# Optimization experiments

Hardware: AMD Instinct MI355X
Metric: run time of the kernel (lower is better)

## Reference

```python
import jax, jax.numpy as jnp
import numpy as np
from jax import lax

B, CIN, H, W = 64, 3, 64, 64
HID = 128          # hidden_dim == embedding_dim
K = 1024           # num_embeddings
BETA = 0.25        # commitment cost


def _conv(x, w, b, stride):
    # torch Conv2d, padding=0, NCHW / OIHW weights
    y = lax.conv_general_dilated(x, w, (stride, stride), 'VALID',
                                 dimension_numbers=('NCHW', 'OIHW', 'NCHW'))
    return y + b[None, :, None, None]


def _conv_transpose(x, w, b, stride):
    # torch ConvTranspose2d, padding=0; w is [Cin, Cout, kh, kw] (torch layout)
    kh, kw = w.shape[2], w.shape[3]
    w2 = jnp.flip(w, (2, 3)).transpose(1, 0, 2, 3)  # -> OIHW, spatially flipped
    y = lax.conv_general_dilated(x, w2, (1, 1),
                                 [(kh - 1, kh - 1), (kw - 1, kw - 1)],
                                 lhs_dilation=(stride, stride),
                                 dimension_numbers=('NCHW', 'OIHW', 'NCHW'))
    return y + b[None, :, None, None]


def setup_inputs() -> dict:
    key = jax.random.key(0)
    ks = jax.random.split(key, 10)
    s = 0.05
    return {
        'x':      jax.random.normal(ks[0], (B, CIN, H, W), jnp.float32),
        'enc_w1': jax.random.normal(ks[1], (HID, CIN, 4, 4), jnp.float32) * s,
        'enc_b1': jnp.zeros((HID,), jnp.float32),
        'enc_w2': jax.random.normal(ks[2], (HID, HID, 2, 2), jnp.float32) * s,
        'enc_b2': jnp.zeros((HID,), jnp.float32),
        'codebook': jax.random.uniform(ks[3], (K, HID), jnp.float32,
                                       minval=-1.0 / K, maxval=1.0 / K),
        'dec_w1': jax.random.normal(ks[4], (HID, HID, 2, 2), jnp.float32) * s,
        'dec_b1': jnp.zeros((HID,), jnp.float32),
        'dec_w2': jax.random.normal(ks[5], (HID, CIN, 4, 4), jnp.float32) * s,
        'dec_b2': jnp.zeros((CIN,), jnp.float32),
    }


def reference(x, enc_w1, enc_b1, enc_w2, enc_b2, codebook,
              dec_w1, dec_b1, dec_w2, dec_b2):
    # ---- encoder ----
    z = jax.nn.relu(_conv(x, enc_w1, enc_b1, 2))
    z = jax.nn.relu(_conv(z, enc_w2, enc_b2, 1))   # [B, HID, 30, 30]

    # ---- vector quantizer (faithful to torch reshape semantics) ----
    D = HID
    flat = z.reshape(-1, D)                        # [N, D], C-order rows
    # squared euclidean distances (argmin identical to torch.cdist argmin)
    d2 = (jnp.sum(flat * flat, axis=1, keepdims=True)
          - 2.0 * flat @ codebook.T
          + jnp.sum(codebook * codebook, axis=1)[None, :])  # [N, K]
    idx = jnp.argmin(d2, axis=1)                   # [N]
    quantized = codebook[idx].reshape(z.shape)

    e_latent = jnp.mean((lax.stop_gradient(quantized) - z) ** 2)
    q_latent = jnp.mean((quantized - lax.stop_gradient(z)) ** 2)
    loss = q_latent + BETA * e_latent

    q_st = z + lax.stop_gradient(quantized - z)    # straight-through

    n = flat.shape[0]
    avg_probs = jnp.zeros((K,), z.dtype).at[idx].add(1.0) / n
    perplexity = jnp.exp(-jnp.sum(avg_probs * jnp.log(avg_probs + 1e-10)))

    # ---- decoder ----
    y = jax.nn.relu(_conv_transpose(q_st, dec_w1, dec_b1, 1))
    x_recon = _conv_transpose(y, dec_w2, dec_b2, 2)  # [B, 3, 64, 64]
    return x_recon, loss, perplexity
```

## Files before the change

### kernel.cpp

```cpp
#include <hip/hip_runtime.h>

#define B_    64
#define CIN_  3
#define HW_   64
#define HID_  128
#define K_    1024
#define H1_   31
#define H2_   30
#define NROWS_ 57600
#define NELEM_ 7372800

typedef __bf16 bf16_t;
typedef __attribute__((ext_vector_type(8))) __bf16 bf16x8;
typedef __attribute__((ext_vector_type(4))) float f32x4;
typedef __attribute__((ext_vector_type(16))) float f32x16;

__global__ __launch_bounds__(256) void wprep_k(const float* __restrict__ ew1,
    const float* __restrict__ ew2, const float* __restrict__ dw1,
    const float* __restrict__ dw2, const float* __restrict__ cb,
    bf16_t* __restrict__ wc1, bf16_t* __restrict__ wc2,
    bf16_t* __restrict__ wd1, bf16_t* __restrict__ wt2,
    bf16_t* __restrict__ cbb, float* __restrict__ cnorm,
    unsigned* __restrict__ hist, float* __restrict__ sse) {
  int id = blockIdx.x * 256 + threadIdx.x;
  int t = id >> 14, co = (id >> 7) & 127, ci = id & 127;
  wc2[id] = (bf16_t)ew2[(co * 128 + ci) * 4 + t];
  wd1[id] = (bf16_t)dw1[(ci * 128 + co) * 4 + (3 - t)];
  if (id < 8192) {
    int n = id >> 9, k = id & 511;
    int tap = k >> 7, c = k & 127;
    if (n < 12) {
      int nco = n >> 2, ph = (n >> 1) & 1, pw = n & 1;
      int off = (tap >> 1) * 8 + (tap & 1) * 2;
      wt2[id] = (bf16_t)dw2[c * 48 + nco * 16 + ph * 4 + pw + off];
    } else {
      wt2[id] = (bf16_t)0.f;
    }
    int c1 = id >> 6, k1 = id & 63;
    wc1[id] = (bf16_t)(k1 < 48 ? ew1[c1 * 48 + k1] : 0.f);
  }
  if (id < K_) {
    float s0 = 0.f;
    for (int d = 0; d < HID_; d += 4) {
      float4 v = *(const float4*)&cb[id * HID_ + d];
      bf16_t tt[4] = {(bf16_t)v.x, (bf16_t)v.y, (bf16_t)v.z, (bf16_t)v.w};
      *(ushort4*)&((ushort*)cbb)[id * HID_ + d] = *(ushort4*)tt;
      float f0 = (float)tt[0], f1 = (float)tt[1];
      float f2 = (float)tt[2], f3 = (float)tt[3];
      s0 += f0 * f0 + f1 * f1 + f2 * f2 + f3 * f3;
    }
    cnorm[id] = s0;
    hist[id] = 0u;
  }
  if (id == 0) *sse = 0.f;
}

__global__ __launch_bounds__(256, 2) void conv1m_k(const float* __restrict__ x,
    const bf16_t* __restrict__ wc1, const float* __restrict__ bias,
    ushort* __restrict__ z1t) {
  __shared__ __align__(16) bf16_t as_[64 * 72];
  __shared__ __align__(16) bf16_t bs_[128 * 72];
  int b = blockIdx.x >> 4, rt = blockIdx.x & 15;
  int tid = threadIdx.x, wv = tid >> 6, ln = tid & 63;
  const float* xb = x + (size_t)b * 12288;
  #pragma unroll
  for (int it = 0; it < 16; ++it) {
    int e = it * 256 + tid;
    int p = e >> 6, k = e & 63;
    float v = 0.f;
    if (k < 48) {
      int ci = k >> 4, kh = (k >> 2) & 3, kw = k & 3;
      int row = 2 * rt + (p >> 5); if (row > 30) row = 30;
      int col = p & 31;            if (col > 30) col = 30;
      v = xb[ci * 4096 + (2 * row + kh) * 64 + 2 * col + kw];
    }
    as_[p * 72 + k] = (bf16_t)v;
  }
  {
    const float4* wg = (const float4*)wc1;
    #pragma unroll
    for (int it = 0; it < 4; ++it) {
      int fi = it * 256 + tid;
      int co = fi >> 3, k8 = fi & 7;
      *(float4*)&bs_[co * 72 + k8 * 8] = wg[fi];
    }
  }
  __syncthreads();
  int q = ln >> 4, l = ln & 15;
  f32x4 acc8[8];
  #pragma unroll
  for (int c = 0; c < 8; ++c) acc8[c] = (f32x4){0.f, 0.f, 0.f, 0.f};
  bf16x8 af[2];
  #pragma unroll
  for (int kk = 0; kk < 2; ++kk)
    af[kk] = *(const bf16x8*)&as_[(wv * 16 + l) * 72 + kk * 32 + q * 8];
  #pragma unroll
  for (int cot = 0; cot < 8; ++cot) {
    #pragma unroll
    for (int kk = 0; kk < 2; ++kk) {
      bf16x8 bf = *(const bf16x8*)&bs_[(cot * 16 + l) * 72 + kk * 32 + q * 8];
      acc8[cot] = __builtin_amdgcn_mfma_f32_16x16x32_bf16(af[kk], bf,
                                                          acc8[cot], 0, 0, 0);
    }
  }
  #pragma unroll
  for (int cot = 0; cot < 8; ++cot) {
    int co = cot * 16 + l;
    float bv = bias[co];
    #pragma unroll
    for (int r = 0; r < 4; ++r) {
      int pos = wv * 16 + q * 4 + r;
      int prow = 2 * rt + (pos >> 5), pcol = pos & 31;
      if (prow < 31 && pcol < 31) {
        float v = fmaxf(acc8[cot][r] + bv, 0.f);
        bf16_t h = (bf16_t)v;
        z1t[((size_t)(b * 1024 + prow * 32 + pcol)) * 128 + co] = *(ushort*)&h;
      }
    }
  }
}

__global__ __launch_bounds__(256, 2) void conv2m_k(const bf16_t* __restrict__ z1t,
    const bf16_t* __restrict__ wc2, const float* __restrict__ bias,
    ushort* __restrict__ zbuf) {
  __shared__ __align__(16) bf16_t as_[98 * 136];
  __shared__ __align__(16) bf16_t bs_[128 * 136];
  int blk = blockIdx.x;
  int b = blk / 15, rt = blk % 15;
  int tid = threadIdx.x, wv = tid >> 6, ln = tid & 63;
  const float4* src = (const float4*)(z1t + ((size_t)b * 1024 + rt * 64) * 128);
  #pragma unroll
  for (int s = 0; s < 7; ++s) {
    int f = s * 256 + tid;
    if (f < 1568) {
      int lp = f >> 4, c16 = f & 15;
      *(float4*)&as_[lp * 136 + c16 * 8] = src[f];
    }
  }
  int m = wv * 16 + (ln & 15), q = ln >> 4;
  f32x4 acc8[8];
  #pragma unroll
  for (int c = 0; c < 8; ++c) acc8[c] = (f32x4){0.f, 0.f, 0.f, 0.f};
  const float4* w4 = (const float4*)wc2;
  #pragma unroll
  for (int t = 0; t < 4; ++t) {
    __syncthreads();
    #pragma unroll
    for (int s = 0; s < 8; ++s) {
      int f = s * 256 + tid;
      int co = f >> 4, c16 = f & 15;
      *(float4*)&bs_[co * 136 + c16 * 8] = w4[t * 2048 + f];
    }
    __syncthreads();
    int off = (t >> 1) * 32 + (t & 1);
    bf16x8 af[4];
    #pragma unroll
    for (int kk = 0; kk < 4; ++kk)
      af[kk] = *(const bf16x8*)&as_[(m + off) * 136 + kk * 32 + q * 8];
    #pragma unroll
    for (int cot = 0; cot < 8; ++cot) {
      #pragma unroll
      for (int kk = 0; kk < 4; ++kk) {
        bf16x8 bf = *(const bf16x8*)&bs_[(cot * 16 + (ln & 15)) * 136 +
                                         kk * 32 + q * 8];
        acc8[cot] = __builtin_amdgcn_mfma_f32_16x16x32_bf16(af[kk], bf,
                                                            acc8[cot], 0, 0, 0);
      }
    }
  }
  #pragma unroll
  for (int cot = 0; cot < 8; ++cot) {
    int co = cot * 16 + (ln & 15);
    float bv = bias[co];
    #pragma unroll
    for (int r = 0; r < 4; ++r) {
      int mo = wv * 16 + q * 4 + r;
      int ocol = mo & 31;
      if (ocol < 30) {
        int orow = rt * 2 + (mo >> 5);
        float v = fmaxf(acc8[cot][r] + bv, 0.f);
        bf16_t h = (bf16_t)v;
        zbuf[(size_t)(b * HID_ + co) * 900 + orow * 30 + ocol] = *(ushort*)&h;
      }
    }
  }
}

__global__ __launch_bounds__(256, 2) void vq1_k(const bf16_t* __restrict__ zb,
    const bf16_t* __restrict__ cbb, const float* __restrict__ cnorm,
    int* __restrict__ idxArr, unsigned* __restrict__ hist,
    float* __restrict__ sse) {
  __shared__ __align__(16) bf16_t zs[64 * 136];
  __shared__ __align__(16) bf16_t cbs[128 * 136];
  __shared__ float cns[K_];
  __shared__ unsigned long long red2[128];
  int n0 = blockIdx.x * 64;
  int tid = threadIdx.x;
  int wv = tid >> 6, ln = tid & 63;
  {
    const float4* zg4 = (const float4*)(zb + (size_t)n0 * HID_);
    #pragma unroll
    for (int s = 0; s < 4; ++s) {
      int f = s * 256 + tid;
      int row = f >> 4, seg = f & 15;
      *(float4*)&zs[row * 136 + seg * 8] = zg4[f];
    }
    ((float4*)cns)[tid] = ((const float4*)cnorm)[tid];
  }
  __syncthreads();
  int mt = wv & 1, npair = wv >> 1;
  int lr = ln & 31, lh = ln >> 5;
  bf16x8 afr[8];
  #pragma unroll
  for (int ks = 0; ks < 8; ++ks)
    afr[ks] = *(const bf16x8*)&zs[(mt * 32 + lr) * 136 + ks * 16 + lh * 8];
  unsigned long long best[16];
  #pragma unroll
  for (int r = 0; r < 16; ++r) best[r] = ~0ull;
  const float4* cg4 = (const float4*)cbb;
  for (int c0 = 0; c0 < K_; c0 += 128) {
    __syncthreads();
    #pragma unroll
    for (int s = 0; s < 8; ++s) {
      int f = s * 256 + tid;
      int code = f >> 4, seg = f & 15;
      *(float4*)&cbs[code * 136 + seg * 8] = cg4[(c0 + code) * 16 + seg];
    }
    __syncthreads();
    #pragma unroll
    for (int nt2 = 0; nt2 < 2; ++nt2) {
      int nt = npair * 2 + nt2;
      f32x16 acc = {0.f, 0.f, 0.f, 0.f, 0.f, 0.f, 0.f, 0.f,
                    0.f, 0.f, 0.f, 0.f, 0.f, 0.f, 0.f, 0.f};
      #pragma unroll
      for (int ks = 0; ks < 8; ++ks) {
        bf16x8 bfr = *(const bf16x8*)&cbs[(nt * 32 + lr) * 136 +
                                          ks * 16 + lh * 8];
        acc = __builtin_amdgcn_mfma_f32_32x32x16_bf16(afr[ks], bfr, acc,
                                                      0, 0, 0);
      }
      int code = c0 + nt * 32 + lr;
      float cn = cns[code];
      unsigned long long lc = (unsigned)code;
      #pragma unroll
      for (int r = 0; r < 16; ++r) {
        float dist = cn - 2.f * acc[r];
        unsigned u = __float_as_uint(dist);
        u = (u & 0x80000000u) ? ~u : (u | 0x80000000u);
        unsigned long long p = ((unsigned long long)u << 32) | lc;
        if (p < best[r]) best[r] = p;
      }
    }
  }
  #pragma unroll
  for (int r = 0; r < 16; ++r) {
    unsigned long long b = best[r];
    #pragma unroll
    for (int o = 16; o > 0; o >>= 1) {
      unsigned long long ob = __shfl_xor(b, o, 64);
      if (ob < b) b = ob;
    }
    best[r] = b;
  }
  if (lr == 0) {
    #pragma unroll
    for (int r = 0; r < 16; ++r)
      red2[((mt * 2 + npair) * 2 + lh) * 16 + r] = best[r];
  }
  __syncthreads();
  if (tid < 64) {
    int fmt = tid >> 5, r32 = tid & 31;
    int half = (r32 >> 2) & 1;
    int reg = (r32 & 3) | (((r32 >> 3) & 3) << 2);
    unsigned long long b0 = red2[((fmt * 2 + 0) * 2 + half) * 16 + reg];
    unsigned long long b1 = red2[((fmt * 2 + 1) * 2 + half) * 16 + reg];
    unsigned long long b = (b1 < b0) ? b1 : b0;
    int bi = (int)(b & 0xffffffffu);
    idxArr[n0 + tid] = bi;
    atomicAdd(&hist[bi], 1u);
    unsigned hi = (unsigned)(b >> 32);
    unsigned orig = (hi & 0x80000000u) ? (hi & 0x7fffffffu) : ~hi;
    float dmin = __uint_as_float(orig);
    float zn = 0.f;
    #pragma unroll
    for (int s = 0; s < 16; ++s) {
      bf16x8 v = *(const bf16x8*)&zs[tid * 136 + s * 8];
      #pragma unroll
      for (int e = 0; e < 8; ++e) {
        float fv = (float)v[e];
        zn = fmaf(fv, fv, zn);
      }
    }
    float se = zn + dmin;
    #pragma unroll
    for (int o = 32; o > 0; o >>= 1) se += __shfl_down(se, o, 64);
    if (tid == 0) atomicAdd(sse, se);
  }
}

__global__ __launch_bounds__(256) void tqz_k(const bf16_t* __restrict__ cbb,
    const int* __restrict__ idxArr, ushort* __restrict__ qt) {
  __shared__ ushort t[60 * 128];
  int bid = blockIdx.x, tid = threadIdx.x;
  if (bid < 960) {
    int b = bid / 15, st = bid % 15;
    int s0 = st * 60;
    #pragma unroll
    for (int it = 0; it < 8; ++it) {
      int task = it * 256 + tid;
      if (task < 1920) {
        int sc = task >> 7, c = task & 127;
        int f = b * 115200 + c * 900 + s0 + sc * 4;
        int n = f >> 7, d = f & 127;
        int k = idxArr[n];
        ushort4 v = *(const ushort4*)((const ushort*)cbb + k * 128 + d);
        t[(sc * 4 + 0) * 128 + c] = v.x;
        t[(sc * 4 + 1) * 128 + c] = v.y;
        t[(sc * 4 + 2) * 128 + c] = v.z;
        t[(sc * 4 + 3) * 128 + c] = v.w;
      }
    }
    __syncthreads();
    #pragma unroll
    for (int it = 0; it < 4; ++it) {
      int task = it * 256 + tid;
      if (task < 960) {
        int sl = task >> 4, c16 = task & 15;
        int s = s0 + sl;
        int h = s / 30, w = s - h * 30;
        int p = (h + 1) * 32 + (w + 1);
        *(uint4*)&qt[((size_t)(b * 1024 + p)) * 128 + c16 * 8] =
            *(uint4*)&t[sl * 128 + c16 * 8];
      }
    }
  } else {
    int zb_ = (bid - 960) * 4;
    uint4 zz = {0u, 0u, 0u, 0u};
    for (int e = tid; e < 4 * 124 * 16; e += 256) {
      int bb = zb_ + e / (124 * 16);
      int rem = e % (124 * 16);
      int pe = rem >> 4, s16 = rem & 15;
      int p;
      if (pe < 32) p = pe;
      else if (pe < 64) p = 31 * 32 + (pe - 32);
      else {
        int idx = pe - 64;
        p = (1 + (idx >> 1)) * 32 + ((idx & 1) ? 31 : 0);
      }
      *(uint4*)&qt[((size_t)(bb * 1024 + p)) * 128 + s16 * 8] = zz;
    }
  }
}

__global__ __launch_bounds__(256, 2) void convt1m_k(const bf16_t* __restrict__ qt,
    const bf16_t* __restrict__ wd1, const float* __restrict__ bias,
    ushort* __restrict__ yt) {
  __shared__ __align__(16) bf16_t as_[98 * 136];
  __shared__ __align__(16) bf16_t bs_[128 * 136];
  int blk = blockIdx.x;
  int b = blk >> 4, rt = blk & 15;
  int tid = threadIdx.x, wv = tid >> 6, ln = tid & 63;
  {
    uint4 zz = {0u, 0u, 0u, 0u};
    ushort* ytb = yt + (size_t)b * 1156 * 128;
    int nrows = (rt < 15) ? 2 : 1;
    int r0 = 2 * rt + 1;
    for (int e = tid; e < nrows * 48; e += 256) {
      int rr = e / 48, rem = e % 48, cc = rem / 16, s16 = rem % 16;
      int col = (cc == 0) ? 0 : (cc == 1 ? 32 : 33);
      *(uint4*)&ytb[((size_t)((r0 + rr) * 34 + col)) * 128 + s16 * 8] = zz;
    }
    if (rt == 0)
      for (int e = tid; e < 34 * 16; e += 256)
        *(uint4*)&ytb[((size_t)(e >> 4)) * 128 + (e & 15) * 8] = zz;
    if (rt == 15)
      for (int e = tid; e < 2 * 34 * 16; e += 256) {
        int rr = 32 + e / 544, rem = e % 544;
        *(uint4*)&ytb[((size_t)(rr * 34 + (rem >> 4))) * 128 + (rem & 15) * 8]
            = zz;
      }
  }
  const float4* src = (const float4*)(qt + (size_t)b * 1024 * 128);
  #pragma unroll
  for (int s = 0; s < 7; ++s) {
    int f = s * 256 + tid;
    if (f < 1568) {
      int lp = f >> 4, c16 = f & 15;
      int gr = rt * 64 + lp;
      if (gr > 1023) gr = 1023;
      *(float4*)&as_[lp * 136 + c16 * 8] = src[gr * 16 + c16];
    }
  }
  int m = wv * 16 + (ln & 15), q = ln >> 4;
  f32x4 acc8[8];
  #pragma unroll
  for (int c = 0; c < 8; ++c) acc8[c] = (f32x4){0.f, 0.f, 0.f, 0.f};
  const float4* w4 = (const float4*)wd1;
  #pragma unroll
  for (int t = 0; t < 4; ++t) {
    __syncthreads();
    #pragma unroll
    for (int s = 0; s < 8; ++s) {
      int f = s * 256 + tid;
      int co = f >> 4, c16 = f & 15;
      *(float4*)&bs_[co * 136 + c16 * 8] = w4[t * 2048 + f];
    }
    __syncthreads();
    int off = (t >> 1) * 32 + (t & 1);
    bf16x8 af[4];
    #pragma unroll
    for (int kk = 0; kk < 4; ++kk)
      af[kk] = *(const bf16x8*)&as_[(m + off) * 136 + kk * 32 + q * 8];
    #pragma unroll
    for (int cot = 0; cot < 8; ++cot) {
      #pragma unroll
      for (int kk = 0; kk < 4; ++kk) {
        bf16x8 bf = *(const bf16x8*)&bs_[(cot * 16 + (ln & 15)) * 136 +
                                         kk * 32 + q * 8];
        acc8[cot] = __builtin_amdgcn_mfma_f32_16x16x32_bf16(af[kk], bf,
                                                            acc8[cot], 0, 0, 0);
      }
    }
  }
  #pragma unroll
  for (int cot = 0; cot < 8; ++cot) {
    int co = cot * 16 + (ln & 15);
    float bv = bias[co];
    #pragma unroll
    for (int r = 0; r < 4; ++r) {
      int mo = wv * 16 + q * 4 + r;
      int orow = rt * 2 + (mo >> 5), ocol = mo & 31;
      if (orow < 31 && ocol < 31) {
        float v = fmaxf(acc8[cot][r] + bv, 0.f);
        bf16_t h = (bf16_t)v;
        yt[((size_t)b * 1156 + (orow + 1) * 34 + (ocol + 1)) * 128 + co] =
            *(ushort*)&h;
      }
    }
  }
}

__global__ __launch_bounds__(256, 2) void convt2m_k(const bf16_t* __restrict__ yt,
    const bf16_t* __restrict__ wt2, const float* __restrict__ bias,
    const unsigned* __restrict__ hist, const float* __restrict__ sse,
    float* __restrict__ out) {
  __shared__ __align__(16) bf16_t as_[128 * 136];
  __shared__ float redf[256];
  int b = blockIdx.x >> 4, rt = blockIdx.x & 15;
  int tid = threadIdx.x, wv = tid >> 6, ln = tid & 63;
  const float4* src = (const float4*)(yt + ((size_t)b * 1156 + rt * 68) * 128);
  #pragma unroll
  for (int s = 0; s < 8; ++s) {
    int f = s * 256 + tid;
    int lp = f >> 4, c16 = f & 15;
    *(float4*)&as_[lp * 136 + c16 * 8] = src[f];
  }
  __syncthreads();
  int mloc = wv * 16 + (ln & 15), q = ln >> 4;
  int qh = mloc >> 5, qw = mloc & 31;
  int base = (qh + 1) * 34 + qw + 1;
  f32x4 acc = {0.f, 0.f, 0.f, 0.f};
  #pragma unroll
  for (int kc = 0; kc < 16; ++kc) {
    int tap = kc >> 2;
    int toff = (tap & 1) + (tap >> 1) * 34;
    bf16x8 af = *(const bf16x8*)&as_[(base - toff) * 136 +
                                     (kc & 3) * 32 + q * 8];
    bf16x8 bf = *(const bf16x8*)&wt2[(size_t)(ln & 15) * 512 + kc * 32 + q * 8];
    acc = __builtin_amdgcn_mfma_f32_16x16x32_bf16(af, bf, acc, 0, 0, 0);
  }
  __syncthreads();
  float* bb = (float*)as_;
  #pragma unroll
  for (int r = 0; r < 4; ++r)
    bb[(wv * 16 + q * 4 + r) * 16 + (ln & 15)] = acc[r];
  __syncthreads();
  if (tid < 192) {
    int row_id = tid >> 4;
    int co = row_id >> 2, ohoff = row_id & 3;
    int qhl = ohoff >> 1, ph = ohoff & 1;
    float bv = bias[co];
    int ow0 = (tid & 15) * 4;
    float tmp[4];
    #pragma unroll
    for (int e = 0; e < 4; ++e) {
      int ow = ow0 + e;
      tmp[e] = bb[(qhl * 32 + (ow >> 1)) * 16 + co * 4 + ph * 2 + (ow & 1)]
               + bv;
    }
    *(float4*)&out[((size_t)(b * 3 + co)) * 4096 + (rt * 4 + ohoff) * 64 + ow0]
        = *(float4*)tmp;
  }
  if (blockIdx.x == 0) {
    float e = 0.f;
    for (int k = tid; k < K_; k += 256) {
      float p = (float)hist[k] * (1.0f / (float)NROWS_);
      e += p * logf(p + 1e-10f);
    }
    redf[tid] = e;
    __syncthreads();
    #pragma unroll
    for (int t = 128; t > 0; t >>= 1) {
      if (tid < t) redf[tid] += redf[tid + t];
      __syncthreads();
    }
    if (tid == 0) {
      out[786432] = 1.25f * (*sse) * (1.0f / (float)NELEM_);
      out[786433] = expf(-redf[0]);
    }
  }
}

extern "C" void kernel_launch(void* const* d_in, const int* in_sizes, int n_in,
                              void* d_out, int out_size, void* d_ws,
                              size_t ws_size, hipStream_t stream) {
  (void)in_sizes; (void)n_in; (void)out_size; (void)ws_size;
  const float* x   = (const float*)d_in[0];
  const float* ew1 = (const float*)d_in[1];
  const float* eb1 = (const float*)d_in[2];
  const float* ew2 = (const float*)d_in[3];
  const float* eb2 = (const float*)d_in[4];
  const float* cb  = (const float*)d_in[5];
  const float* dw1 = (const float*)d_in[6];
  const float* db1 = (const float*)d_in[7];
  const float* dw2 = (const float*)d_in[8];
  const float* db2 = (const float*)d_in[9];
  float* out = (float*)d_out;
  char* ws = (char*)d_ws;

  ushort*   yt    = (ushort*)(ws);
  bf16_t*   z1t   = (bf16_t*)(ws + 65175552);
  bf16_t*   qt    = (bf16_t*)(ws + 65175552);
  ushort*   zbuf  = (ushort*)(ws + 81985536);
  bf16_t*   cbb   = (bf16_t*)(ws + 96731136);
  bf16_t*   wc2   = (bf16_t*)(ws + 96993280);
  bf16_t*   wd1   = (bf16_t*)(ws + 97124352);
  int*      idxArr= (int*)(ws + 97255424);
  unsigned* hist  = (unsigned*)(ws + 97485824);
  float*    cnorm = (float*)(ws + 97489920);
  float*    sse   = (float*)(ws + 97494016);
  bf16_t*   wt2   = (bf16_t*)(ws + 97497088);
  bf16_t*   wc1   = (bf16_t*)(ws + 97513472);

  wprep_k<<<dim3(256), dim3(256), 0, stream>>>(ew1, ew2, dw1, dw2, cb,
                                               wc1, wc2, wd1, wt2,
                                               cbb, cnorm, hist, sse);
  conv1m_k<<<dim3(1024), dim3(256), 0, stream>>>(x, wc1, eb1, (ushort*)z1t);
  conv2m_k<<<dim3(960), dim3(256), 0, stream>>>(z1t, wc2, eb2, zbuf);
  vq1_k<<<dim3(900), dim3(256), 0, stream>>>((const bf16_t*)zbuf, cbb, cnorm,
                                             idxArr, hist, sse);
  tqz_k<<<dim3(976), dim3(256), 0, stream>>>(cbb, idxArr, (ushort*)qt);
  convt1m_k<<<dim3(1024), dim3(256), 0, stream>>>(qt, wd1, db1, yt);
  convt2m_k<<<dim3(1024), dim3(256), 0, stream>>>((const bf16_t*)yt, wt2, db2,
                                                  hist, sse, out);
}
```

Baseline: 230.4 us.

## Enlarge VQ tile to 128 rows, prefetch codebook into registers, simplify argmin

The VQ distance kernel now handles 128 rows per block instead of 64, so each codebook tile loaded into shared memory is reused across twice as many rows, and the grid halves to 450 blocks. The next codebook chunk is prefetched into registers while the current one is computed. The 64-bit packed argmin is replaced by a float max of dot minus half the code norm, with explicit index tie-breaking. The cost is more registers per thread and more shared memory, and the fewer, larger blocks may leave some compute units idle.

```diff
diff --git a/kernel.cpp b/kernel.cpp
--- a/kernel.cpp
+++ b/kernel.cpp
@@ -190,111 +190,133 @@
     const bf16_t* __restrict__ cbb, const float* __restrict__ cnorm,
     int* __restrict__ idxArr, unsigned* __restrict__ hist,
     float* __restrict__ sse) {
-  __shared__ __align__(16) bf16_t zs[64 * 136];
+  __shared__ __align__(16) bf16_t zs[128 * 136];
   __shared__ __align__(16) bf16_t cbs[128 * 136];
   __shared__ float cns[K_];
-  __shared__ unsigned long long red2[128];
-  int n0 = blockIdx.x * 64;
+  __shared__ float redS[256];
+  __shared__ int   redI[256];
+  int n0 = blockIdx.x * 128;
   int tid = threadIdx.x;
   int wv = tid >> 6, ln = tid & 63;
+  int lr = ln & 31, lh = ln >> 5;
+  int mtp = wv >> 1, ntp = wv & 1;
   {
     const float4* zg4 = (const float4*)(zb + (size_t)n0 * HID_);
     #pragma unroll
-    for (int s = 0; s < 4; ++s) {
-      int f = s * 256 + tid;
-      int row = f >> 4, seg = f & 15;
-      *(float4*)&zs[row * 136 + seg * 8] = zg4[f];
-    }
-    ((float4*)cns)[tid] = ((const float4*)cnorm)[tid];
-  }
-  __syncthreads();
-  int mt = wv & 1, npair = wv >> 1;
-  int lr = ln & 31, lh = ln >> 5;
-  bf16x8 afr[8];
-  #pragma unroll
-  for (int ks = 0; ks < 8; ++ks)
-    afr[ks] = *(const bf16x8*)&zs[(mt * 32 + lr) * 136 + ks * 16 + lh * 8];
-  unsigned long long best[16];
-  #pragma unroll
-  for (int r = 0; r < 16; ++r) best[r] = ~0ull;
-  const float4* cg4 = (const float4*)cbb;
-  for (int c0 = 0; c0 < K_; c0 += 128) {
-    __syncthreads();
-    #pragma unroll
     for (int s = 0; s < 8; ++s) {
       int f = s * 256 + tid;
-      int code = f >> 4, seg = f & 15;
-      *(float4*)&cbs[code * 136 + seg * 8] = cg4[(c0 + code) * 16 + seg];
-    }
-    __syncthreads();
+      *(float4*)&zs[(f >> 4) * 136 + (f & 15) * 8] = zg4[f];
+    }
+    float4 cv = ((const float4*)cnorm)[tid];
+    cv.x *= 0.5f; cv.y *= 0.5f; cv.z *= 0.5f; cv.w *= 0.5f;
+    ((float4*)cns)[tid] = cv;
+  }
+  const float4* cg4 = (const float4*)cbb;
+  float4 pf[8];
+  #pragma unroll
+  for (int s = 0; s < 8; ++s) pf[s] = cg4[s * 256 + tid];
+  __syncthreads();
+  bf16x8 af0[8], af1[8];
+  #pragma unroll
+  for (int ks = 0; ks < 8; ++ks) {
+    af0[ks] = *(const bf16x8*)&zs[(mtp * 64 + lr) * 136 + ks * 16 + lh * 8];
+    af1[ks] = *(const bf16x8*)&zs[(mtp * 64 + 32 + lr) * 136 +
+                                  ks * 16 + lh * 8];
+  }
+  float bS0[16], bS1[16];
+  int   bI0[16], bI1[16];
+  #pragma unroll
+  for (int r = 0; r < 16; ++r) {
+    bS0[r] = -3.4e38f; bS1[r] = -3.4e38f; bI0[r] = 0; bI1[r] = 0;
+  }
+  for (int c0 = 0; c0 < K_; c0 += 128) {
+    __syncthreads();
+    #pragma unroll
+    for (int s = 0; s < 8; ++s) {
+      int f = s * 256 + tid;
+      *(float4*)&cbs[(f >> 4) * 136 + (f & 15) * 8] = pf[s];
+    }
+    __syncthreads();
+    if (c0 + 128 < K_) {
+      #pragma unroll
+      for (int s = 0; s < 8; ++s)
+        pf[s] = cg4[(c0 + 128) * 16 + s * 256 + tid];
+    }
     #pragma unroll
     for (int nt2 = 0; nt2 < 2; ++nt2) {
-      int nt = npair * 2 + nt2;
-      f32x16 acc = {0.f, 0.f, 0.f, 0.f, 0.f, 0.f, 0.f, 0.f,
-                    0.f, 0.f, 0.f, 0.f, 0.f, 0.f, 0.f, 0.f};
+      int nt = ntp * 2 + nt2;
+      int code = c0 + nt * 32 + lr;
+      float hcn = cns[code];
+      f32x16 a0 = {0.f, 0.f, 0.f, 0.f, 0.f, 0.f, 0.f, 0.f,
+                   0.f, 0.f, 0.f, 0.f, 0.f, 0.f, 0.f, 0.f};
+      f32x16 a1 = {0.f, 0.f, 0.f, 0.f, 0.f, 0.f, 0.f, 0.f,
+                   0.f, 0.f, 0.f, 0.f, 0.f, 0.f, 0.f, 0.f};
       #pragma unroll
       for (int ks = 0; ks < 8; ++ks) {
         bf16x8 bfr = *(const bf16x8*)&cbs[(nt * 32 + lr) * 136 +
                                           ks * 16 + lh * 8];
-        acc = __builtin_amdgcn_mfma_f32_32x32x16_bf16(afr[ks], bfr, acc,
-                                                      0, 0, 0);
-      }
-      int code = c0 + nt * 32 + lr;
-      float cn = cns[code];
-      unsigned long long lc = (unsigned)code;
+        a0 = __builtin_amdgcn_mfma_f32_32x32x16_bf16(af0[ks], bfr, a0, 0, 0, 0);
+        a1 = __builtin_amdgcn_mfma_f32_32x32x16_bf16(af1[ks], bfr, a1, 0, 0, 0);
+      }
       #pragma unroll
       for (int r = 0; r < 16; ++r) {
-        float dist = cn - 2.f * acc[r];
-        unsigned u = __float_as_uint(dist);
-        u = (u & 0x80000000u) ? ~u : (u | 0x80000000u);
-        unsigned long long p = ((unsigned long long)u << 32) | lc;
-        if (p < best[r]) best[r] = p;
+        float s0 = a0[r] - hcn;
+        if (s0 > bS0[r]) { bS0[r] = s0; bI0[r] = code; }
+        float s1 = a1[r] - hcn;
+        if (s1 > bS1[r]) { bS1[r] = s1; bI1[r] = code; }
       }
     }
   }
   #pragma unroll
   for (int r = 0; r < 16; ++r) {
-    unsigned long long b = best[r];
+    float s0 = bS0[r]; int i0 = bI0[r];
+    float s1 = bS1[r]; int i1 = bI1[r];
     #pragma unroll
     for (int o = 16; o > 0; o >>= 1) {
-      unsigned long long ob = __shfl_xor(b, o, 64);
-      if (ob < b) b = ob;
-    }
-    best[r] = b;
+      float os = __shfl_xor(s0, o, 64); int oi = __shfl_xor(i0, o, 64);
+      if (os > s0 || (os == s0 && oi < i0)) { s0 = os; i0 = oi; }
+      os = __shfl_xor(s1, o, 64); oi = __shfl_xor(i1, o, 64);
+      if (os > s1 || (os == s1 && oi < i1)) { s1 = os; i1 = oi; }
+    }
+    bS0[r] = s0; bI0[r] = i0; bS1[r] = s1; bI1[r] = i1;
   }
   if (lr == 0) {
-    #pragma unroll
-    for (int r = 0; r < 16; ++r)
-      red2[((mt * 2 + npair) * 2 + lh) * 16 + r] = best[r];
+    int base0 = ((mtp * 2 + 0) * 4 + ntp * 2 + lh) * 16;
+    int base1 = ((mtp * 2 + 1) * 4 + ntp * 2 + lh) * 16;
+    #pragma unroll
+    for (int r = 0; r < 16; ++r) {
+      redS[base0 + r] = bS0[r]; redI[base0 + r] = bI0[r];
+      redS[base1 + r] = bS1[r]; redI[base1 + r] = bI1[r];
+    }
   }
   __syncthreads();
-  if (tid < 64) {
-    int fmt = tid >> 5, r32 = tid & 31;
+  if (tid < 128) {
+    int mtg = tid >> 5, r32 = tid & 31;
     int half = (r32 >> 2) & 1;
     int reg = (r32 & 3) | (((r32 >> 3) & 3) << 2);
-    unsigned long long b0 = red2[((fmt * 2 + 0) * 2 + half) * 16 + reg];
-    unsigned long long b1 = red2[((fmt * 2 + 1) * 2 + half) * 16 + reg];
-    unsigned long long b = (b1 < b0) ? b1 : b0;
-    int bi = (int)(b & 0xffffffffu);
+    int e0 = (mtg * 4 + half) * 16 + reg;
+    int e1 = (mtg * 4 + 2 + half) * 16 + reg;
+    float s0 = redS[e0], s1 = redS[e1];
+    int b0 = redI[e0], b1 = redI[e1];
+    bool t = (s1 > s0) || (s1 == s0 && b1 < b0);
+    float sbest = t ? s1 : s0;
+    int bi = t ? b1 : b0;
     idxArr[n0 + tid] = bi;
     atomicAdd(&hist[bi], 1u);
-    unsigned hi = (unsigned)(b >> 32);
-    unsigned orig = (hi & 0x80000000u) ? (hi & 0x7fffffffu) : ~hi;
-    float dmin = __uint_as_float(orig);
     float zn = 0.f;
     #pragma unroll
-    for (int s = 0; s < 16; ++s) {
-      bf16x8 v = *(const bf16x8*)&zs[tid * 136 + s * 8];
+    for (int sg = 0; sg < 16; ++sg) {
+      bf16x8 v = *(const bf16x8*)&zs[tid * 136 + sg * 8];
       #pragma unroll
       for (int e = 0; e < 8; ++e) {
         float fv = (float)v[e];
         zn = fmaf(fv, fv, zn);
       }
     }
-    float se = zn + dmin;
+    float se = zn - 2.f * sbest;
     #pragma unroll
     for (int o = 32; o > 0; o >>= 1) se += __shfl_down(se, o, 64);
-    if (tid == 0) atomicAdd(sse, se);
+    if (ln == 0) atomicAdd(sse, se);
   }
 }
 
@@ -547,7 +569,7 @@
                                                cbb, cnorm, hist, sse);
   conv1m_k<<<dim3(1024), dim3(256), 0, stream>>>(x, wc1, eb1, (ushort*)z1t);
   conv2m_k<<<dim3(960), dim3(256), 0, stream>>>(z1t, wc2, eb2, zbuf);
-  vq1_k<<<dim3(900), dim3(256), 0, stream>>>((const bf16_t*)zbuf, cbb, cnorm,
+  vq1_k<<<dim3(450), dim3(256), 0, stream>>>((const bf16_t*)zbuf, cbb, cnorm,
                                              idxArr, hist, sse);
   tqz_k<<<dim3(976), dim3(256), 0, stream>>>(cbb, idxArr, (ushort*)qt);
   convt1m_k<<<dim3(1024), dim3(256), 0, stream>>>(qt, wd1, db1, yt);
```

Result: slower. 248.0 us (+7.6%).

## Restructure VQ argmin to stream codebook from global into registers, drop LDS tiles

Applied to the files above, without the earlier changes.

The VQ kernel now gives each wave 32 full rows against all 1024 codes. Codebook fragments are loaded straight from global (L2-resident) into registers with double buffering, replacing the LDS staging and its block barriers. The accumulator is seeded with -0.5*||c||^2 so argmin becomes an argmax on float score plus index, dropping the 64-bit packed compare. Blocks handle 128 rows, so half as many blocks each do more work, which could reduce occupancy or parallelism and puts more load on the cache through repeated codebook reads.

```diff
diff --git a/kernel.cpp b/kernel.cpp
--- a/kernel.cpp
+++ b/kernel.cpp
@@ -190,111 +190,113 @@
     const bf16_t* __restrict__ cbb, const float* __restrict__ cnorm,
     int* __restrict__ idxArr, unsigned* __restrict__ hist,
     float* __restrict__ sse) {
-  __shared__ __align__(16) bf16_t zs[64 * 136];
-  __shared__ __align__(16) bf16_t cbs[128 * 136];
   __shared__ float cns[K_];
-  __shared__ unsigned long long red2[128];
-  int n0 = blockIdx.x * 64;
+  __shared__ float redS[128];
+  __shared__ int   redI[128];
+  int n0 = blockIdx.x * 128;
   int tid = threadIdx.x;
   int wv = tid >> 6, ln = tid & 63;
+  int lr = ln & 31, lh = ln >> 5;
   {
-    const float4* zg4 = (const float4*)(zb + (size_t)n0 * HID_);
-    #pragma unroll
-    for (int s = 0; s < 4; ++s) {
-      int f = s * 256 + tid;
-      int row = f >> 4, seg = f & 15;
-      *(float4*)&zs[row * 136 + seg * 8] = zg4[f];
-    }
-    ((float4*)cns)[tid] = ((const float4*)cnorm)[tid];
-  }
+    float4 cv = ((const float4*)cnorm)[tid];
+    cv.x *= -0.5f; cv.y *= -0.5f; cv.z *= -0.5f; cv.w *= -0.5f;
+    ((float4*)cns)[tid] = cv;
+  }
+  const ushort* za = (const ushort*)zb +
+                     ((size_t)(n0 + wv * 32 + lr)) * 128 + lh * 8;
+  bf16x8 af[8];
+  #pragma unroll
+  for (int ks = 0; ks < 8; ++ks) af[ks] = *(const bf16x8*)(za + ks * 16);
+  const ushort* cbB = (const ushort*)cbb + (size_t)lr * 128 + lh * 8;
+  bf16x8 bf0[8], bf1[8];
+  #pragma unroll
+  for (int ks = 0; ks < 8; ++ks) bf0[ks] = *(const bf16x8*)(cbB + ks * 16);
+  float bS[16];
+  int   bI[16];
+  #pragma unroll
+  for (int r = 0; r < 16; ++r) { bS[r] = -3.4e38f; bI[r] = 0; }
   __syncthreads();
-  int mt = wv & 1, npair = wv >> 1;
-  int lr = ln & 31, lh = ln >> 5;
-  bf16x8 afr[8];
-  #pragma unroll
-  for (int ks = 0; ks < 8; ++ks)
-    afr[ks] = *(const bf16x8*)&zs[(mt * 32 + lr) * 136 + ks * 16 + lh * 8];
-  unsigned long long best[16];
-  #pragma unroll
-  for (int r = 0; r < 16; ++r) best[r] = ~0ull;
-  const float4* cg4 = (const float4*)cbb;
-  for (int c0 = 0; c0 < K_; c0 += 128) {
-    __syncthreads();
-    #pragma unroll
-    for (int s = 0; s < 8; ++s) {
-      int f = s * 256 + tid;
-      int code = f >> 4, seg = f & 15;
-      *(float4*)&cbs[code * 136 + seg * 8] = cg4[(c0 + code) * 16 + seg];
-    }
-    __syncthreads();
-    #pragma unroll
-    for (int nt2 = 0; nt2 < 2; ++nt2) {
-      int nt = npair * 2 + nt2;
-      f32x16 acc = {0.f, 0.f, 0.f, 0.f, 0.f, 0.f, 0.f, 0.f,
-                    0.f, 0.f, 0.f, 0.f, 0.f, 0.f, 0.f, 0.f};
-      #pragma unroll
-      for (int ks = 0; ks < 8; ++ks) {
-        bf16x8 bfr = *(const bf16x8*)&cbs[(nt * 32 + lr) * 136 +
-                                          ks * 16 + lh * 8];
-        acc = __builtin_amdgcn_mfma_f32_32x32x16_bf16(afr[ks], bfr, acc,
+  for (int nt = 0; nt < 32; nt += 2) {
+    {
+      const ushort* cbn = cbB + (size_t)(nt + 1) * 4096;
+      #pragma unroll
+      for (int ks = 0; ks < 8; ++ks)
+        bf1[ks] = *(const bf16x8*)(cbn + ks * 16);
+    }
+    {
+      float hv = cns[nt * 32 + lr];
+      f32x16 acc;
+      #pragma unroll
+      for (int r = 0; r < 16; ++r) acc[r] = hv;
+      #pragma unroll
+      for (int ks = 0; ks < 8; ++ks)
+        acc = __builtin_amdgcn_mfma_f32_32x32x16_bf16(af[ks], bf0[ks], acc,
                                                       0, 0, 0);
-      }
-      int code = c0 + nt * 32 + lr;
-      float cn = cns[code];
-      unsigned long long lc = (unsigned)code;
-      #pragma unroll
-      for (int r = 0; r < 16; ++r) {
-        float dist = cn - 2.f * acc[r];
-        unsigned u = __float_as_uint(dist);
-        u = (u & 0x80000000u) ? ~u : (u | 0x80000000u);
-        unsigned long long p = ((unsigned long long)u << 32) | lc;
-        if (p < best[r]) best[r] = p;
-      }
+      int code = nt * 32 + lr;
+      #pragma unroll
+      for (int r = 0; r < 16; ++r)
+        if (acc[r] > bS[r]) { bS[r] = acc[r]; bI[r] = code; }
+    }
+    if (nt + 2 < 32) {
+      const ushort* cbn = cbB + (size_t)(nt + 2) * 4096;
+      #pragma unroll
+      for (int ks = 0; ks < 8; ++ks)
+        bf0[ks] = *(const bf16x8*)(cbn + ks * 16);
+    }
+    {
+      float hv = cns[(nt + 1) * 32 + lr];
+      f32x16 acc;
+      #pragma unroll
+      for (int r = 0; r < 16; ++r) acc[r] = hv;
+      #pragma unroll
+      for (int ks = 0; ks < 8; ++ks)
+        acc = __builtin_amdgcn_mfma_f32_32x32x16_bf16(af[ks], bf1[ks], acc,
+                                                      0, 0, 0);
+      int code = (nt + 1) * 32 + lr;
+      #pragma unroll
+      for (int r = 0; r < 16; ++r)
+        if (acc[r] > bS[r]) { bS[r] = acc[r]; bI[r] = code; }
     }
   }
   #pragma unroll
   for (int r = 0; r < 16; ++r) {
-    unsigned long long b = best[r];
+    float s = bS[r]; int i = bI[r];
     #pragma unroll
     for (int o = 16; o > 0; o >>= 1) {
-      unsigned long long ob = __shfl_xor(b, o, 64);
-      if (ob < b) b = ob;
-    }
-    best[r] = b;
+      float os = __shfl_xor(s, o, 64); int oi = __shfl_xor(i, o, 64);
+      if (os > s || (os == s && oi < i)) { s = os; i = oi; }
+    }
+    bS[r] = s; bI[r] = i;
   }
   if (lr == 0) {
     #pragma unroll
-    for (int r = 0; r < 16; ++r)
-      red2[((mt * 2 + npair) * 2 + lh) * 16 + r] = best[r];
+    for (int r = 0; r < 16; ++r) {
+      int row = (r & 3) + 4 * lh + 8 * (r >> 2);
+      redS[wv * 32 + row] = bS[r];
+      redI[wv * 32 + row] = bI[r];
+    }
   }
   __syncthreads();
-  if (tid < 64) {
-    int fmt = tid >> 5, r32 = tid & 31;
-    int half = (r32 >> 2) & 1;
-    int reg = (r32 & 3) | (((r32 >> 3) & 3) << 2);
-    unsigned long long b0 = red2[((fmt * 2 + 0) * 2 + half) * 16 + reg];
-    unsigned long long b1 = red2[((fmt * 2 + 1) * 2 + half) * 16 + reg];
-    unsigned long long b = (b1 < b0) ? b1 : b0;
-    int bi = (int)(b & 0xffffffffu);
+  if (tid < 128) {
+    int bi = redI[tid];
+    float sbest = redS[tid];
     idxArr[n0 + tid] = bi;
     atomicAdd(&hist[bi], 1u);
-    unsigned hi = (unsigned)(b >> 32);
-    unsigned orig = (hi & 0x80000000u) ? (hi & 0x7fffffffu) : ~hi;
-    float dmin = __uint_as_float(orig);
+    const ushort* zr = (const ushort*)zb + (size_t)(n0 + tid) * 128;
     float zn = 0.f;
     #pragma unroll
-    for (int s = 0; s < 16; ++s) {
-      bf16x8 v = *(const bf16x8*)&zs[tid * 136 + s * 8];
+    for (int sg = 0; sg < 16; ++sg) {
+      bf16x8 v = *(const bf16x8*)(zr + sg * 8);
       #pragma unroll
       for (int e = 0; e < 8; ++e) {
         float fv = (float)v[e];
         zn = fmaf(fv, fv, zn);
       }
     }
-    float se = zn + dmin;
+    float se = zn - 2.f * sbest;
     #pragma unroll
     for (int o = 32; o > 0; o >>= 1) se += __shfl_down(se, o, 64);
-    if (tid == 0) atomicAdd(sse, se);
+    if (ln == 0) atomicAdd(sse, se);
   }
 }
 
@@ -547,7 +549,7 @@
                                                cbb, cnorm, hist, sse);
   conv1m_k<<<dim3(1024), dim3(256), 0, stream>>>(x, wc1, eb1, (ushort*)z1t);
   conv2m_k<<<dim3(960), dim3(256), 0, stream>>>(z1t, wc2, eb2, zbuf);
-  vq1_k<<<dim3(900), dim3(256), 0, stream>>>((const bf16_t*)zbuf, cbb, cnorm,
+  vq1_k<<<dim3(450), dim3(256), 0, stream>>>((const bf16_t*)zbuf, cbb, cnorm,
                                              idxArr, hist, sse);
   tqz_k<<<dim3(976), dim3(256), 0, stream>>>(cbb, idxArr, (ushort*)qt);
   convt1m_k<<<dim3(1024), dim3(256), 0, stream>>>(qt, wd1, db1, yt);
```

After: 259.8 us. 1.13x slower.
